# Kernel optimization log

Hardware: AMD Instinct MI355X
Metric: run time of the kernel (lower is better)

## Reference

```python
import jax, jax.numpy as jnp
import numpy as np

EMBED = 2048
HEADS = 32
HEAD_DIM = EMBED // HEADS
Q_BITS = 4
Q_MAX = 2 ** (Q_BITS - 1) - 1  # 7
DECOMP = 8
CHUNK = 256


def _sym_qdq(x, scale):
    # sym_quant followed by sym_dequant (float32 math, clamp to [-8, 7])
    s = jnp.clip(jnp.abs(scale), 1e-9, None)
    return jnp.clip(jnp.round(x / s), -(Q_MAX + 1), Q_MAX) * s


def _quant_weight(w):
    # per-output-channel symmetric int4 quant-dequant of weight [out, in]
    w = w.astype(jnp.float32)
    s = jnp.max(jnp.abs(w), axis=-1, keepdims=True) / Q_MAX
    return _sym_qdq(w, s)


def _chunk_decompose(x2d):
    """Tender chunked activation quantization.
    Splits rows into chunks of CHUNK, subtracts per-chunk channel bias,
    groups channels into DECOMP scale groups by their column max, and
    applies per-group int4 quant-dequant. Vectorized over the DECOMP groups
    (the masks partition channels, so a per-channel scale gather is exact).
    """
    T, H = x2d.shape
    chunks = (T + CHUNK - 1) // CHUNK
    pad = chunks * CHUNK - T
    xp = jnp.pad(x2d, ((0, pad), (0, 0))).reshape(chunks, CHUNK, H).astype(jnp.float32)
    ch_bias = (jnp.max(xp, axis=1, keepdims=True) + jnp.min(xp, axis=1, keepdims=True)) / 2
    xz = xp - ch_bias                                   # [chunks, CHUNK, H]
    tmax = jnp.max(jnp.abs(xz), axis=(1, 2))            # [chunks]
    cmax = jnp.max(jnp.abs(xz), axis=1)                 # [chunks, H]
    # thresholds t_i = tmax / 2^(DECOMP-1-i), ascending in i
    thr = tmax[:, None] / (2.0 ** jnp.arange(DECOMP - 1, -1, -1, dtype=jnp.float32))
    # group index: i=0 if cmax<=t0, else first i with t_{i-1} < cmax <= t_i
    idx = jnp.sum(cmax[:, :, None] > thr[:, None, : DECOMP - 1], axis=-1)  # [chunks, H]
    scale = tmax[:, None] / (2.0 ** (DECOMP - 1 - idx).astype(jnp.float32)) / Q_MAX
    result = _sym_qdq(xz, scale[:, None, :])            # [chunks, CHUNK, H]
    return result, ch_bias, T


def reference(hidden_states, q_weight, k_weight, v_weight, o_weight,
              q_bias, k_bias, v_bias, o_bias):
    bsz, tgt, H = hidden_states.shape
    # int4 dequantized weights, transposed for right-multiply
    WQ = _quant_weight(q_weight).T
    WK = _quant_weight(k_weight).T
    WV = _quant_weight(v_weight).T
    WO = _quant_weight(o_weight).T

    result, ch_bias, n = _chunk_decompose(hidden_states.reshape(bsz * tgt, H))

    def proj(w_orig, w_dq_t, b):
        # bias-corrected dequant GEMM: per-chunk channel bias uses the
        # ORIGINAL (fp) weight, quantized residual uses the int4 weight
        y = result @ w_dq_t + ch_bias @ w_orig.astype(jnp.float32).T
        return y.reshape(-1, H)[:n] + b

    scaling = HEAD_DIM ** -0.5
    Q = (proj(q_weight, WQ, q_bias) * scaling).reshape(bsz, tgt, HEADS, HEAD_DIM)
    K = proj(k_weight, WK, k_bias).reshape(bsz, tgt, HEADS, HEAD_DIM)
    V = proj(v_weight, WV, v_bias).reshape(bsz, tgt, HEADS, HEAD_DIM)

    # quant_mha == False path: plain attention
    attn = jnp.einsum('bqhd,bkhd->bhqk', Q, K)
    probs = jax.nn.softmax(attn, axis=-1)
    ctx = jnp.einsum('bhqk,bkhd->bqhd', probs, V).reshape(bsz * tgt, H)

    # output projection through the same chunked quant pipeline
    r2, cb2, n2 = _chunk_decompose(ctx)
    out = (r2 @ WO + cb2 @ o_weight.astype(jnp.float32).T).reshape(-1, H)[:n2] + o_bias
    return out.reshape(bsz, tgt, H)


def setup_inputs() -> dict:
    key = jax.random.key(0)
    ks = jax.random.split(key, 10)
    B, T = 2, 1024
    inp = {
        'hidden_states': jax.random.normal(ks[0], (B, T, EMBED), dtype=jnp.float32),
        'q_weight': jax.random.normal(ks[1], (EMBED, EMBED), dtype=jnp.float32) * 0.02,
        'k_weight': jax.random.normal(ks[2], (EMBED, EMBED), dtype=jnp.float32) * 0.02,
        'v_weight': jax.random.normal(ks[3], (EMBED, EMBED), dtype=jnp.float32) * 0.02,
        'o_weight': jax.random.normal(ks[4], (EMBED, EMBED), dtype=jnp.float32) * 0.02,
        'q_bias': jax.random.normal(ks[5], (EMBED,), dtype=jnp.float32) * 0.02,
        'k_bias': jax.random.normal(ks[6], (EMBED,), dtype=jnp.float32) * 0.02,
        'v_bias': jax.random.normal(ks[7], (EMBED,), dtype=jnp.float32) * 0.02,
        'o_bias': jax.random.normal(ks[8], (EMBED,), dtype=jnp.float32) * 0.02,
    }
    return inp
```

## Files before the change

### kernel.cpp

```cpp
#include <hip/hip_runtime.h>
#include <hip/hip_bf16.h>

typedef unsigned short u16;
typedef __attribute__((ext_vector_type(8))) short bs8;
typedef __attribute__((ext_vector_type(4))) float fx4;
typedef __attribute__((ext_vector_type(4))) float f4_t;

#define HDIM 2048
#define NCH 8

__device__ inline u16 f2bf(float f) {
  __hip_bfloat16 h = __float2bfloat16(f);
  return __builtin_bit_cast(u16, h);
}
__device__ inline float bf2f(u16 u) {
  __hip_bfloat16 h = __builtin_bit_cast(__hip_bfloat16, u);
  return __bfloat162float(h);
}
__device__ inline float pow2i(int e) {
  return __builtin_bit_cast(float, (unsigned)((127 + e) << 23));
}
__device__ inline void gld_lds16(const void* g, void* l) {
  __builtin_amdgcn_global_load_lds((const __attribute__((address_space(1))) void*)g,
                                   (__attribute__((address_space(3))) void*)l, 16, 0, 0);
}

__global__ __launch_bounds__(256) void k_wquant_cbw(
    const float* __restrict__ w0, const float* __restrict__ w1,
    const float* __restrict__ w2, const float* __restrict__ bias,
    u16* __restrict__ wq, float* __restrict__ sw, float* __restrict__ cbw,
    int NC) {
  int o = blockIdx.x, t = threadIdx.x;
  const float* w = (o < 2048) ? w0 : ((o < 4096) ? w1 : w2);
  const float* wrow = w + (size_t)(o & 2047) * HDIM;
  const f4_t* row4 = (const f4_t*)wrow;
  f4_t x0 = row4[2 * t], x1 = row4[2 * t + 1];
  float am = 0.f;
#pragma unroll
  for (int j = 0; j < 4; j++) { am = fmaxf(am, fabsf(x0[j])); am = fmaxf(am, fabsf(x1[j])); }
#pragma unroll
  for (int m = 1; m < 64; m <<= 1) am = fmaxf(am, __shfl_xor(am, m));
  __shared__ float red[4];
  if ((t & 63) == 0) red[t >> 6] = am;
  __syncthreads();
  am = fmaxf(fmaxf(red[0], red[1]), fmaxf(red[2], red[3]));
  float s = fmaxf(am / 7.0f, 1e-9f);
  if (t == 0) sw[o] = s;
  bs8 ov;
#pragma unroll
  for (int j = 0; j < 4; j++) {
    float q0 = fminf(fmaxf(rintf(x0[j] / s), -8.f), 7.f);
    float q1 = fminf(fmaxf(rintf(x1[j] / s), -8.f), 7.f);
    ov[j]     = (short)f2bf(q0);
    ov[j + 4] = (short)f2bf(q1);
  }
  ((bs8*)(wq + (size_t)o * HDIM))[t] = ov;
  float acc[NCH];
#pragma unroll
  for (int c = 0; c < NCH; c++) {
    const f4_t* bc = (const f4_t*)(bias + (size_t)c * HDIM);
    f4_t b0 = bc[2 * t], b1 = bc[2 * t + 1];
    float a = 0.f;
#pragma unroll
    for (int j = 0; j < 4; j++) a += x0[j] * b0[j] + x1[j] * b1[j];
    acc[c] = a;
  }
  __shared__ float redc[NCH][4];
#pragma unroll
  for (int c = 0; c < NCH; c++) {
    float a = acc[c];
#pragma unroll
    for (int m = 1; m < 64; m <<= 1) a += __shfl_xor(a, m);
    if ((t & 63) == 0) redc[c][t >> 6] = a;
  }
  __syncthreads();
  if (t < NCH) cbw[t * NC + o] = redc[t][0] + redc[t][1] + redc[t][2] + redc[t][3];
}

__global__ __launch_bounds__(256) void k_stats(const float* __restrict__ x,
                                               float* __restrict__ biasO,
                                               float* __restrict__ cmaxO) {
  int ch = blockIdx.x >> 3;
  int c = ((blockIdx.x & 7) << 8) + threadIdx.x;
  const float* base = x + (size_t)ch * 256 * HDIM + c;
  float mx = -1e30f, mn = 1e30f;
  for (int r = 0; r < 256; r++) { float v = base[(size_t)r * HDIM]; mx = fmaxf(mx, v); mn = fminf(mn, v); }
  float bi = (mx + mn) * 0.5f;
  biasO[ch * HDIM + c] = bi;
  cmaxO[ch * HDIM + c] = fmaxf(mx - bi, bi - mn);
}

__global__ __launch_bounds__(256) void k_tscale(const float* __restrict__ cmax,
                                                float* __restrict__ scaleO,
                                                float* __restrict__ e2O,
                                                float* __restrict__ tcO) {
  int ch = blockIdx.x, t = threadIdx.x;
  const float* cr = cmax + ch * HDIM;
  float v[8];
  float mx = 0.f;
#pragma unroll
  for (int i = 0; i < 8; i++) { v[i] = cr[i * 256 + t]; mx = fmaxf(mx, v[i]); }
#pragma unroll
  for (int m = 1; m < 64; m <<= 1) mx = fmaxf(mx, __shfl_xor(mx, m));
  __shared__ float red[4];
  __shared__ float tms;
  if ((t & 63) == 0) red[t >> 6] = mx;
  __syncthreads();
  if (t == 0) tms = fmaxf(fmaxf(red[0], red[1]), fmaxf(red[2], red[3]));
  __syncthreads();
  float tmax = tms;
  if (t == 0) tcO[ch] = (tmax / 7.0f) * pow2i(-7);
#pragma unroll
  for (int i = 0; i < 8; i++) {
    int idx = 0;
#pragma unroll
    for (int k = 0; k < 7; k++) idx += (v[i] > tmax * pow2i(k - 7)) ? 1 : 0;
    float s = (tmax * pow2i(idx - 7)) / 7.0f;
    scaleO[ch * HDIM + i * 256 + t] = fmaxf(s, 1e-9f);
    e2O[ch * HDIM + i * 256 + t] = pow2i(idx);
  }
}

__global__ __launch_bounds__(256) void k_qdq(const float* __restrict__ x,
                                             const float* __restrict__ bias,
                                             const float* __restrict__ scale,
                                             const float* __restrict__ e2,
                                             u16* __restrict__ out) {
  int row = blockIdx.x, t = threadIdx.x;
  int ch = row >> 8;
  const f4_t* xr = (const f4_t*)(x + (size_t)row * HDIM);
  const f4_t* br = (const f4_t*)(bias + (size_t)ch * HDIM);
  const f4_t* sr = (const f4_t*)(scale + (size_t)ch * HDIM);
  const f4_t* er = (const f4_t*)(e2 + (size_t)ch * HDIM);
  f4_t x0 = xr[2 * t], x1 = xr[2 * t + 1];
  f4_t b0 = br[2 * t], b1 = br[2 * t + 1];
  f4_t s0 = sr[2 * t], s1 = sr[2 * t + 1];
  f4_t e0 = er[2 * t], e1 = er[2 * t + 1];
  bs8 ov;
#pragma unroll
  for (int j = 0; j < 4; j++) {
    float q0 = fminf(fmaxf(rintf((x0[j] - b0[j]) / s0[j]), -8.f), 7.f);
    ov[j] = (short)f2bf(q0 * e0[j]);
    float q1 = fminf(fmaxf(rintf((x1[j] - b1[j]) / s1[j]), -8.f), 7.f);
    ov[j + 4] = (short)f2bf(q1 * e1[j]);
  }
  ((bs8*)(out + (size_t)row * HDIM))[t] = ov;
}

__global__ __launch_bounds__(256) void k_gemm(
    const u16* __restrict__ A, const u16* __restrict__ B,
    float* __restrict__ o0, float* __restrict__ o1, float* __restrict__ o2,
    const float* __restrict__ cbw, int NC,
    const float* __restrict__ bb0, const float* __restrict__ bb1,
    const float* __restrict__ bb2,
    const float* __restrict__ tc, const float* __restrict__ sw,
    float scl0, float scl1, float scl2) {
  __shared__ u16 smA[128 * 32];
  __shared__ u16 smB[128 * 32];
  int tid = threadIdx.x;
  int wave = tid >> 6, lane = tid & 63;
  int wr = wave >> 1, wc = wave & 1;
  int row0 = blockIdx.y * 128, col0 = blockIdx.x * 128;
  int mat = col0 >> 11;
  float* out = (mat == 0) ? o0 : ((mat == 1) ? o1 : o2);
  const float* bias = (mat == 0) ? bb0 : ((mat == 1) ? bb1 : bb2);
  float scl = (mat == 0) ? scl0 : ((mat == 1) ? scl1 : scl2);
  int chunk = row0 >> 8;
  fx4 zz = {0.f, 0.f, 0.f, 0.f};
  fx4 acc[4][4];
#pragma unroll
  for (int m = 0; m < 4; m++)
#pragma unroll
    for (int n = 0; n < 4; n++) acc[m][n] = zz;

  int offB = wave * 1024 + lane * 16;
  int sr0 = offB >> 6;
  int sr1 = sr0 + 64;
  int sk = (lane & 3) << 3;
  char* ldsA0 = (char*)smA + wave * 1024;
  char* ldsA1 = (char*)smA + 4096 + wave * 1024;
  char* ldsB0 = (char*)smB + wave * 1024;
  char* ldsB1 = (char*)smB + 4096 + wave * 1024;
  const u16* Ab = A + (size_t)row0 * HDIM;
  const u16* Bb = B + (size_t)col0 * HDIM;

  int arow = wr * 64 + (lane & 15);
  int brow = wc * 64 + (lane & 15);
  int kByte = (lane >> 4) << 4;

  for (int kt = 0; kt < HDIM / 32; kt++) {
    int kb = kt * 32 + sk;
    gld_lds16(Ab + (size_t)sr0 * HDIM + kb, ldsA0);
    gld_lds16(Ab + (size_t)sr1 * HDIM + kb, ldsA1);
    gld_lds16(Bb + (size_t)sr0 * HDIM + kb, ldsB0);
    gld_lds16(Bb + (size_t)sr1 * HDIM + kb, ldsB1);
    __syncthreads();
    bs8 af[4], bfr[4];
#pragma unroll
    for (int m = 0; m < 4; m++)
      af[m] = *(const bs8*)((const char*)smA + (size_t)((arow + m * 16) * 64 + kByte));
#pragma unroll
    for (int n = 0; n < 4; n++)
      bfr[n] = *(const bs8*)((const char*)smB + (size_t)((brow + n * 16) * 64 + kByte));
#pragma unroll
    for (int m = 0; m < 4; m++)
#pragma unroll
      for (int n = 0; n < 4; n++)
        acc[m][n] = __builtin_amdgcn_mfma_f32_16x16x32_bf16(af[m], bfr[n], acc[m][n], 0, 0, 0);
    __syncthreads();
  }
  float tcv = tc[chunk];
  int colb = col0 + wc * 64 + (lane & 15);
  int rowb = row0 + wr * 64 + ((lane >> 4) << 2);
#pragma unroll
  for (int m = 0; m < 4; m++) {
#pragma unroll
    for (int n = 0; n < 4; n++) {
      int colg = colb + n * 16;
      int colL = colg - (mat << 11);
      float sc = tcv * sw[colg];
      float cb = cbw[chunk * NC + colg] + bias[colL];
#pragma unroll
      for (int j = 0; j < 4; j++) {
        int row = rowb + m * 16 + j;
        out[(size_t)row * HDIM + colL] = (acc[m][n][j] * sc + cb) * scl;
      }
    }
  }
}

__global__ __launch_bounds__(256) void k_gemm_sk(const u16* __restrict__ A,
                                                 const u16* __restrict__ B,
                                                 float* __restrict__ pbuf) {
  __shared__ u16 smA[128 * 32];
  __shared__ u16 smB[128 * 32];
  int tid = threadIdx.x;
  int wave = tid >> 6, lane = tid & 63;
  int wr = wave >> 1, wc = wave & 1;
  int row0 = blockIdx.y * 128, col0 = blockIdx.x * 128;
  int z = blockIdx.z;
  float* out = pbuf + (size_t)z * HDIM * HDIM;
  fx4 zz = {0.f, 0.f, 0.f, 0.f};
  fx4 acc[4][4];
#pragma unroll
  for (int m = 0; m < 4; m++)
#pragma unroll
    for (int n = 0; n < 4; n++) acc[m][n] = zz;

  int offB = wave * 1024 + lane * 16;
  int sr0 = offB >> 6;
  int sr1 = sr0 + 64;
  int sk = (lane & 3) << 3;
  char* ldsA0 = (char*)smA + wave * 1024;
  char* ldsA1 = (char*)smA + 4096 + wave * 1024;
  char* ldsB0 = (char*)smB + wave * 1024;
  char* ldsB1 = (char*)smB + 4096 + wave * 1024;
  const u16* Ab = A + (size_t)row0 * HDIM;
  const u16* Bb = B + (size_t)col0 * HDIM;

  int arow = wr * 64 + (lane & 15);
  int brow = wc * 64 + (lane & 15);
  int kByte = (lane >> 4) << 4;

  for (int kt = z * 32; kt < z * 32 + 32; kt++) {
    int kb = kt * 32 + sk;
    gld_lds16(Ab + (size_t)sr0 * HDIM + kb, ldsA0);
    gld_lds16(Ab + (size_t)sr1 * HDIM + kb, ldsA1);
    gld_lds16(Bb + (size_t)sr0 * HDIM + kb, ldsB0);
    gld_lds16(Bb + (size_t)sr1 * HDIM + kb, ldsB1);
    __syncthreads();
    bs8 af[4], bfr[4];
#pragma unroll
    for (int m = 0; m < 4; m++)
      af[m] = *(const bs8*)((const char*)smA + (size_t)((arow + m * 16) * 64 + kByte));
#pragma unroll
    for (int n = 0; n < 4; n++)
      bfr[n] = *(const bs8*)((const char*)smB + (size_t)((brow + n * 16) * 64 + kByte));
#pragma unroll
    for (int m = 0; m < 4; m++)
#pragma unroll
      for (int n = 0; n < 4; n++)
        acc[m][n] = __builtin_amdgcn_mfma_f32_16x16x32_bf16(af[m], bfr[n], acc[m][n], 0, 0, 0);
    __syncthreads();
  }
  int colb = col0 + wc * 64 + (lane & 15);
  int rowb = row0 + wr * 64 + ((lane >> 4) << 2);
#pragma unroll
  for (int m = 0; m < 4; m++)
#pragma unroll
    for (int n = 0; n < 4; n++)
#pragma unroll
      for (int j = 0; j < 4; j++)
        out[(size_t)(rowb + m * 16 + j) * HDIM + colb + n * 16] = acc[m][n][j];
}

__global__ __launch_bounds__(256) void k_fin(const float* __restrict__ p0,
                                             const float* __restrict__ p1,
                                             const float* __restrict__ cbw,
                                             const float* __restrict__ bias,
                                             const float* __restrict__ tc,
                                             const float* __restrict__ sw,
                                             float* __restrict__ out) {
  int row = blockIdx.x, t = threadIdx.x;
  int chunk = row >> 8;
  float tcv = tc[chunk];
  const f4_t* a = (const f4_t*)(p0 + (size_t)row * HDIM);
  const f4_t* b = (const f4_t*)(p1 + (size_t)row * HDIM);
  f4_t* o = (f4_t*)(out + (size_t)row * HDIM);
#pragma unroll
  for (int u = 0; u < 2; u++) {
    f4_t x = a[2 * t + u], y = b[2 * t + u];
    f4_t r;
#pragma unroll
    for (int j = 0; j < 4; j++) {
      int c = (2 * t + u) * 4 + j;
      float sc = tcv * sw[c];
      float cb = cbw[chunk * HDIM + c] + bias[c];
      r[j] = ((x[j] + y[j]) * sc + cb) * 1.0f;
    }
    o[2 * t + u] = r;
  }
}

__global__ __launch_bounds__(256) void k_split(const float* __restrict__ Kf,
                                               const float* __restrict__ Vf,
                                               u16* __restrict__ Khg,
                                               u16* __restrict__ Klg,
                                               u16* __restrict__ Vhg,
                                               u16* __restrict__ Vlg) {
  __shared__ u16 Th[4096], Tl[4096];
  int t = threadIdx.x;
  int ti = blockIdx.x & 15, h = (blockIdx.x >> 4) & 31, b = blockIdx.x >> 9;
  size_t rowStart = (size_t)b * 1024 + ti * 64;
  int colh = h * 64;
  size_t tbase = ((size_t)((b * 32 + h) * 16 + ti)) * 4096;
  int kr = t >> 2, d0 = (t & 3) << 4;
  int xk = (kr & 7) << 3;
  const float* kp = Kf + (rowStart + kr) * HDIM + colh + d0;
  const float* vp = Vf + (rowStart + kr) * HDIM + colh + d0;
  f4_t kv[4], vv[4];
#pragma unroll
  for (int qd = 0; qd < 4; qd++) { kv[qd] = *(const f4_t*)(kp + 4 * qd); vv[qd] = *(const f4_t*)(vp + 4 * qd); }
  bs8 h0, l0, h1, l1;
#pragma unroll
  for (int j = 0; j < 4; j++) {
    float x = kv[0][j]; u16 hh = f2bf(x); h0[j] = (short)hh; l0[j] = (short)f2bf(x - bf2f(hh));
    x = kv[1][j]; hh = f2bf(x); h0[j + 4] = (short)hh; l0[j + 4] = (short)f2bf(x - bf2f(hh));
    x = kv[2][j]; hh = f2bf(x); h1[j] = (short)hh; l1[j] = (short)f2bf(x - bf2f(hh));
    x = kv[3][j]; hh = f2bf(x); h1[j + 4] = (short)hh; l1[j + 4] = (short)f2bf(x - bf2f(hh));
  }
  *(bs8*)(Khg + tbase + kr * 64 + (d0 ^ xk)) = h0;
  *(bs8*)(Klg + tbase + kr * 64 + (d0 ^ xk)) = l0;
  *(bs8*)(Khg + tbase + kr * 64 + ((d0 + 8) ^ xk)) = h1;
  *(bs8*)(Klg + tbase + kr * 64 + ((d0 + 8) ^ xk)) = l1;
#pragma unroll
  for (int qd = 0; qd < 4; qd++)
#pragma unroll
    for (int j = 0; j < 4; j++) {
      int d = d0 + 4 * qd + j;
      float x = vv[qd][j]; u16 hh = f2bf(x);
      int vi = d * 64 + (kr ^ ((d & 7) << 3));
      Th[vi] = hh; Tl[vi] = f2bf(x - bf2f(hh));
    }
  __syncthreads();
  *(bs8*)(Vhg + tbase + t * 16) = *(const bs8*)&Th[t * 16];
  *(bs8*)(Vhg + tbase + t * 16 + 8) = *(const bs8*)&Th[t * 16 + 8];
  *(bs8*)(Vlg + tbase + t * 16) = *(const bs8*)&Tl[t * 16];
  *(bs8*)(Vlg + tbase + t * 16 + 8) = *(const bs8*)&Tl[t * 16 + 8];
}

__global__ __launch_bounds__(256) void k_attn(const float* __restrict__ Q,
                                              const u16* __restrict__ Khg,
                                              const u16* __restrict__ Klg,
                                              const u16* __restrict__ Vhg,
                                              const u16* __restrict__ Vlg,
                                              float* __restrict__ O) {
  __shared__ u16 Kh[64 * 64], Kl[64 * 64];
  __shared__ u16 Vh[64 * 64], Vl[64 * 64];
  int tid = threadIdx.x, wave = tid >> 6, lane = tid & 63;
  int l15 = lane & 15, l4 = lane >> 4;
  int lid = blockIdx.x;
  int xcd = lid & 7, jj = lid >> 3;
  int pair = xcd * 8 + (jj >> 4);
  int qt = jj & 15;
  int h = pair & 31, b = pair >> 5;
  size_t rowStart = (size_t)b * 1024;
  int colh = h * 64;
  int qbase = qt * 64 + wave * 16;
  size_t hbase = (size_t)pair * 16 * 4096;
  u16* Phw = &Kh[wave * 1024];
  u16* Plw = &Kl[wave * 1024];

  bs8 qh[2], ql[2];
#pragma unroll
  for (int kk = 0; kk < 2; kk++) {
    const float* qp = Q + (rowStart + qbase + l15) * HDIM + colh + kk * 32 + (l4 << 3);
    f4_t a0 = *(const f4_t*)qp;
    f4_t a1 = *(const f4_t*)(qp + 4);
#pragma unroll
    for (int j = 0; j < 4; j++) {
      float x = a0[j]; u16 hh = f2bf(x);
      qh[kk][j] = (short)hh; ql[kk][j] = (short)f2bf(x - bf2f(hh));
      x = a1[j]; hh = f2bf(x);
      qh[kk][j + 4] = (short)hh; ql[kk][j + 4] = (short)f2bf(x - bf2f(hh));
    }
  }

  fx4 zz = {0.f, 0.f, 0.f, 0.f};
  fx4 oacc[4];
  float mrun[4], lrun[4];
#pragma unroll
  for (int n = 0; n < 4; n++) oacc[n] = zz;
#pragma unroll
  for (int j = 0; j < 4; j++) { mrun[j] = -1e30f; lrun[j] = 0.f; }

  const u16* garr = (wave == 0) ? Khg : (wave == 1) ? Klg : (wave == 2) ? Vhg : Vlg;
  u16* larr = (wave == 0) ? Kh : (wave == 1) ? Kl : (wave == 2) ? Vh : Vl;

  for (int ti = 0; ti < 16; ti++) {
    const u16* gsrc = garr + hbase + (size_t)ti * 4096 + lane * 8;
#pragma unroll
    for (int seg = 0; seg < 8; seg++)
      gld_lds16(gsrc + seg * 512, larr + seg * 512);
    __syncthreads();

    fx4 sf[4];
#pragma unroll
    for (int n = 0; n < 4; n++) sf[n] = zz;
    __builtin_amdgcn_s_setprio(1);
#pragma unroll
    for (int kk = 0; kk < 2; kk++) {
      int colr = kk * 32 + (l4 << 3);
#pragma unroll
      for (int n = 0; n < 4; n++) {
        int row = n * 16 + l15;
        int ko = row * 64 + (colr ^ ((row & 7) << 3));
        bs8 bh = *(const bs8*)&Kh[ko];
        bs8 bl = *(const bs8*)&Kl[ko];
        sf[n] = __builtin_amdgcn_mfma_f32_16x16x32_bf16(ql[kk], bl, sf[n], 0, 0, 0);
        sf[n] = __builtin_amdgcn_mfma_f32_16x16x32_bf16(ql[kk], bh, sf[n], 0, 0, 0);
        sf[n] = __builtin_amdgcn_mfma_f32_16x16x32_bf16(qh[kk], bl, sf[n], 0, 0, 0);
        sf[n] = __builtin_amdgcn_mfma_f32_16x16x32_bf16(qh[kk], bh, sf[n], 0, 0, 0);
      }
    }
    __builtin_amdgcn_s_setprio(0);
    float corr[4];
#pragma unroll
    for (int j = 0; j < 4; j++) {
      float tm = fmaxf(fmaxf(sf[0][j], sf[1][j]), fmaxf(sf[2][j], sf[3][j]));
#pragma unroll
      for (int msk = 1; msk < 16; msk <<= 1) tm = fmaxf(tm, __shfl_xor(tm, msk));
      float mn = fmaxf(mrun[j], tm);
      corr[j] = __expf(mrun[j] - mn);
      mrun[j] = mn;
      float rs = 0.f;
#pragma unroll
      for (int n = 0; n < 4; n++) { float p = __expf(sf[n][j] - mn); sf[n][j] = p; rs += p; }
#pragma unroll
      for (int msk = 1; msk < 16; msk <<= 1) rs += __shfl_xor(rs, msk);
      lrun[j] = lrun[j] * corr[j] + rs;
    }
#pragma unroll
    for (int n = 0; n < 4; n++)
#pragma unroll
      for (int j = 0; j < 4; j++) oacc[n][j] *= corr[j];
    __syncthreads();
#pragma unroll
    for (int n = 0; n < 4; n++)
#pragma unroll
      for (int j = 0; j < 4; j++) {
        float p = sf[n][j];
        u16 hh = f2bf(p);
        int prow = (l4 << 2) + j;
        int pi = prow * 64 + ((n * 16 + l15) ^ ((prow & 7) << 3));
        Phw[pi] = hh;
        Plw[pi] = f2bf(p - bf2f(hh));
      }
    __builtin_amdgcn_s_setprio(1);
#pragma unroll
    for (int kk = 0; kk < 2; kk++) {
      int colr = kk * 32 + (l4 << 3);
      int ao = l15 * 64 + (colr ^ ((l15 & 7) << 3));
      bs8 pah = *(const bs8*)&Phw[ao];
      bs8 pal = *(const bs8*)&Plw[ao];
#pragma unroll
      for (int n = 0; n < 4; n++) {
        int vrow = n * 16 + l15;
        int vo = vrow * 64 + (colr ^ ((vrow & 7) << 3));
        bs8 vh = *(const bs8*)&Vh[vo];
        bs8 vl = *(const bs8*)&Vl[vo];
        oacc[n] = __builtin_amdgcn_mfma_f32_16x16x32_bf16(pal, vl, oacc[n], 0, 0, 0);
        oacc[n] = __builtin_amdgcn_mfma_f32_16x16x32_bf16(pal, vh, oacc[n], 0, 0, 0);
        oacc[n] = __builtin_amdgcn_mfma_f32_16x16x32_bf16(pah, vl, oacc[n], 0, 0, 0);
        oacc[n] = __builtin_amdgcn_mfma_f32_16x16x32_bf16(pah, vh, oacc[n], 0, 0, 0);
      }
    }
    __builtin_amdgcn_s_setprio(0);
    __syncthreads();
  }
#pragma unroll
  for (int n = 0; n < 4; n++)
#pragma unroll
    for (int j = 0; j < 4; j++)
      O[(rowStart + qbase + (l4 << 2) + j) * HDIM +
        colh + n * 16 + l15] = oacc[n][j] / lrun[j];
}

extern "C" void kernel_launch(void* const* d_in, const int* in_sizes, int n_in,
                              void* d_out, int out_size, void* d_ws, size_t ws_size,
                              hipStream_t stream) {
  const float* hs = (const float*)d_in[0];
  const float* qw = (const float*)d_in[1];
  const float* kw = (const float*)d_in[2];
  const float* vw = (const float*)d_in[3];
  const float* ow = (const float*)d_in[4];
  const float* qb = (const float*)d_in[5];
  const float* kb = (const float*)d_in[6];
  const float* vb = (const float*)d_in[7];
  const float* ob = (const float*)d_in[8];

  char* ws = (char*)d_ws;
  const size_t MB = 1u << 20;
  u16* wqQKV = (u16*)(ws + 0 * MB);
  u16* actA  = (u16*)(ws + 24 * MB);
  u16* Khg   = (u16*)(ws + 0 * MB);
  u16* Klg   = (u16*)(ws + 8 * MB);
  u16* Vhg   = (u16*)(ws + 16 * MB);
  u16* Vlg   = (u16*)(ws + 24 * MB);
  float* p01 = (float*)(ws + 0 * MB);
  float* Qf  = (float*)(ws + 32 * MB);
  float* Kf  = (float*)(ws + 48 * MB);
  float* Vf  = (float*)(ws + 64 * MB);
  u16* actA2 = (u16*)(ws + 48 * MB);
  u16* wqO   = (u16*)(ws + 64 * MB);
  float* sm  = (float*)(ws + 80 * MB);
  float* bias1  = sm;
  float* cmax1  = bias1 + NCH * HDIM;
  float* scale1 = cmax1 + NCH * HDIM;
  float* e2_1   = scale1 + NCH * HDIM;
  float* bias2  = e2_1 + NCH * HDIM;
  float* cmax2  = bias2 + NCH * HDIM;
  float* scale2 = cmax2 + NCH * HDIM;
  float* e2_2   = scale2 + NCH * HDIM;
  float* cbwQKV = e2_2 + NCH * HDIM;
  float* swQKV  = cbwQKV + NCH * 3 * HDIM;
  float* cbwO   = swQKV + 3 * HDIM;
  float* swO    = cbwO + NCH * HDIM;
  float* tc1    = swO + HDIM;
  float* tc2    = tc1 + NCH;
  float* ctx = (float*)d_out;

  k_stats<<<64, 256, 0, stream>>>(hs, bias1, cmax1);
  k_tscale<<<8, 256, 0, stream>>>(cmax1, scale1, e2_1, tc1);
  k_qdq<<<2048, 256, 0, stream>>>(hs, bias1, scale1, e2_1, actA);
  k_wquant_cbw<<<6144, 256, 0, stream>>>(qw, kw, vw, bias1, wqQKV, swQKV, cbwQKV, 3 * HDIM);
  k_gemm<<<dim3(48, 16), 256, 0, stream>>>(actA, wqQKV, Qf, Kf, Vf,
                                           cbwQKV, 3 * HDIM, qb, kb, vb,
                                           tc1, swQKV, 0.125f, 1.0f, 1.0f);
  k_split<<<1024, 256, 0, stream>>>(Kf, Vf, Khg, Klg, Vhg, Vlg);
  k_attn<<<1024, 256, 0, stream>>>(Qf, Khg, Klg, Vhg, Vlg, ctx);
  k_stats<<<64, 256, 0, stream>>>(ctx, bias2, cmax2);
  k_tscale<<<8, 256, 0, stream>>>(cmax2, scale2, e2_2, tc2);
  k_qdq<<<2048, 256, 0, stream>>>(ctx, bias2, scale2, e2_2, actA2);
  k_wquant_cbw<<<2048, 256, 0, stream>>>(ow, ow, ow, bias2, wqO, swO, cbwO, HDIM);
  k_gemm_sk<<<dim3(16, 16, 2), 256, 0, stream>>>(actA2, wqO, p01);
  k_fin<<<2048, 256, 0, stream>>>(p01, p01 + (size_t)HDIM * HDIM,
                                  cbwO, ob, tc2, swO, (float*)d_out);
}
```

Before: 313.2 us.

## Transpose attention MFMAs to keep P in registers and drop LDS round-trip

Swaps MFMA operand order so the score tile comes out transposed. Each lane then holds one query row, so the softmax max/sum needs only two cross-lane shuffles, and the per-row state becomes a single scalar. P is repacked into MFMA operand layout with register shuffles instead of being written to LDS, which removes one __syncthreads per tile and the LDS stores and loads. The output becomes a 16-byte vector store per lane. In exchange it adds many __shfl operations, and correctness depends on the shuffle-based repacking matching the MFMA operand layout exactly.

```diff
diff --git a/kernel.cpp b/kernel.cpp
--- a/kernel.cpp
+++ b/kernel.cpp
@@ -2,9 +2,11 @@
 #include <hip/hip_bf16.h>
 
 typedef unsigned short u16;
+typedef unsigned int u32;
 typedef __attribute__((ext_vector_type(8))) short bs8;
 typedef __attribute__((ext_vector_type(4))) float fx4;
 typedef __attribute__((ext_vector_type(4))) float f4_t;
+typedef __attribute__((ext_vector_type(4))) unsigned int u4_t;
 
 #define HDIM 2048
 #define NCH 8
@@ -388,8 +390,6 @@
   int colh = h * 64;
   int qbase = qt * 64 + wave * 16;
   size_t hbase = (size_t)pair * 16 * 4096;
-  u16* Phw = &Kh[wave * 1024];
-  u16* Plw = &Kl[wave * 1024];
 
   bs8 qh[2], ql[2];
 #pragma unroll
@@ -408,14 +408,16 @@
 
   fx4 zz = {0.f, 0.f, 0.f, 0.f};
   fx4 oacc[4];
-  float mrun[4], lrun[4];
+  float mrun = -1e30f, lrun = 0.f;
 #pragma unroll
   for (int n = 0; n < 4; n++) oacc[n] = zz;
-#pragma unroll
-  for (int j = 0; j < 4; j++) { mrun[j] = -1e30f; lrun[j] = 0.f; }
 
   const u16* garr = (wave == 0) ? Khg : (wave == 1) ? Klg : (wave == 2) ? Vhg : Vlg;
   u16* larr = (wave == 0) ? Kh : (wave == 1) ? Kl : (wave == 2) ? Vh : Vl;
+
+  int srcA = l15 + ((lane & 16) << 1);
+  int srcB = srcA + 16;
+  int hiSel = l4 >> 1;
 
   for (int ti = 0; ti < 16; ti++) {
     const u16* gsrc = garr + hbase + (size_t)ti * 4096 + lane * 8;
@@ -437,73 +439,96 @@
         int ko = row * 64 + (colr ^ ((row & 7) << 3));
         bs8 bh = *(const bs8*)&Kh[ko];
         bs8 bl = *(const bs8*)&Kl[ko];
-        sf[n] = __builtin_amdgcn_mfma_f32_16x16x32_bf16(ql[kk], bl, sf[n], 0, 0, 0);
-        sf[n] = __builtin_amdgcn_mfma_f32_16x16x32_bf16(ql[kk], bh, sf[n], 0, 0, 0);
-        sf[n] = __builtin_amdgcn_mfma_f32_16x16x32_bf16(qh[kk], bl, sf[n], 0, 0, 0);
-        sf[n] = __builtin_amdgcn_mfma_f32_16x16x32_bf16(qh[kk], bh, sf[n], 0, 0, 0);
+        sf[n] = __builtin_amdgcn_mfma_f32_16x16x32_bf16(bl, ql[kk], sf[n], 0, 0, 0);
+        sf[n] = __builtin_amdgcn_mfma_f32_16x16x32_bf16(bh, ql[kk], sf[n], 0, 0, 0);
+        sf[n] = __builtin_amdgcn_mfma_f32_16x16x32_bf16(bl, qh[kk], sf[n], 0, 0, 0);
+        sf[n] = __builtin_amdgcn_mfma_f32_16x16x32_bf16(bh, qh[kk], sf[n], 0, 0, 0);
       }
     }
     __builtin_amdgcn_s_setprio(0);
-    float corr[4];
-#pragma unroll
-    for (int j = 0; j < 4; j++) {
-      float tm = fmaxf(fmaxf(sf[0][j], sf[1][j]), fmaxf(sf[2][j], sf[3][j]));
-#pragma unroll
-      for (int msk = 1; msk < 16; msk <<= 1) tm = fmaxf(tm, __shfl_xor(tm, msk));
-      float mn = fmaxf(mrun[j], tm);
-      corr[j] = __expf(mrun[j] - mn);
-      mrun[j] = mn;
-      float rs = 0.f;
-#pragma unroll
-      for (int n = 0; n < 4; n++) { float p = __expf(sf[n][j] - mn); sf[n][j] = p; rs += p; }
-#pragma unroll
-      for (int msk = 1; msk < 16; msk <<= 1) rs += __shfl_xor(rs, msk);
-      lrun[j] = lrun[j] * corr[j] + rs;
-    }
+    float tm = sf[0][0];
 #pragma unroll
     for (int n = 0; n < 4; n++)
 #pragma unroll
-      for (int j = 0; j < 4; j++) oacc[n][j] *= corr[j];
-    __syncthreads();
+      for (int j = 0; j < 4; j++) tm = fmaxf(tm, sf[n][j]);
+    tm = fmaxf(tm, __shfl_xor(tm, 16));
+    tm = fmaxf(tm, __shfl_xor(tm, 32));
+    float mn = fmaxf(mrun, tm);
+    float corr = __expf(mrun - mn);
+    mrun = mn;
+    float rs = 0.f;
 #pragma unroll
     for (int n = 0; n < 4; n++)
 #pragma unroll
-      for (int j = 0; j < 4; j++) {
-        float p = sf[n][j];
-        u16 hh = f2bf(p);
-        int prow = (l4 << 2) + j;
-        int pi = prow * 64 + ((n * 16 + l15) ^ ((prow & 7) << 3));
-        Phw[pi] = hh;
-        Plw[pi] = f2bf(p - bf2f(hh));
+      for (int j = 0; j < 4; j++) { float p = __expf(sf[n][j] - mn); sf[n][j] = p; rs += p; }
+    rs += __shfl_xor(rs, 16);
+    rs += __shfl_xor(rs, 32);
+    lrun = lrun * corr + rs;
+#pragma unroll
+    for (int n = 0; n < 4; n++)
+#pragma unroll
+      for (int j = 0; j < 4; j++) oacc[n][j] *= corr;
+
+    u32 hiw[4][2], low[4][2];
+#pragma unroll
+    for (int n = 0; n < 4; n++) {
+      u16 hh0 = f2bf(sf[n][0]), hh1 = f2bf(sf[n][1]);
+      u16 hh2 = f2bf(sf[n][2]), hh3 = f2bf(sf[n][3]);
+      u16 ll0 = f2bf(sf[n][0] - bf2f(hh0)), ll1 = f2bf(sf[n][1] - bf2f(hh1));
+      u16 ll2 = f2bf(sf[n][2] - bf2f(hh2)), ll3 = f2bf(sf[n][3] - bf2f(hh3));
+      hiw[n][0] = (u32)hh0 | ((u32)hh1 << 16);
+      hiw[n][1] = (u32)hh2 | ((u32)hh3 << 16);
+      low[n][0] = (u32)ll0 | ((u32)ll1 << 16);
+      low[n][1] = (u32)ll2 | ((u32)ll3 << 16);
+    }
+    bs8 ph[2], pl[2];
+#pragma unroll
+    for (int kkv = 0; kkv < 2; kkv++) {
+      u4_t wh, wl;
+#pragma unroll
+      for (int half = 0; half < 2; half++) {
+        int src = half ? srcB : srcA;
+#pragma unroll
+        for (int pr = 0; pr < 2; pr++) {
+          int a0 = __shfl((int)hiw[2 * kkv][pr], src);
+          int a1 = __shfl((int)hiw[2 * kkv + 1][pr], src);
+          wh[half * 2 + pr] = (u32)(hiSel ? a1 : a0);
+          int b0 = __shfl((int)low[2 * kkv][pr], src);
+          int b1 = __shfl((int)low[2 * kkv + 1][pr], src);
+          wl[half * 2 + pr] = (u32)(hiSel ? b1 : b0);
+        }
       }
+      ph[kkv] = __builtin_bit_cast(bs8, wh);
+      pl[kkv] = __builtin_bit_cast(bs8, wl);
+    }
+
     __builtin_amdgcn_s_setprio(1);
 #pragma unroll
-    for (int kk = 0; kk < 2; kk++) {
-      int colr = kk * 32 + (l4 << 3);
-      int ao = l15 * 64 + (colr ^ ((l15 & 7) << 3));
-      bs8 pah = *(const bs8*)&Phw[ao];
-      bs8 pal = *(const bs8*)&Plw[ao];
+    for (int kkv = 0; kkv < 2; kkv++) {
+      int colr = kkv * 32 + (l4 << 3);
 #pragma unroll
       for (int n = 0; n < 4; n++) {
         int vrow = n * 16 + l15;
         int vo = vrow * 64 + (colr ^ ((vrow & 7) << 3));
         bs8 vh = *(const bs8*)&Vh[vo];
         bs8 vl = *(const bs8*)&Vl[vo];
-        oacc[n] = __builtin_amdgcn_mfma_f32_16x16x32_bf16(pal, vl, oacc[n], 0, 0, 0);
-        oacc[n] = __builtin_amdgcn_mfma_f32_16x16x32_bf16(pal, vh, oacc[n], 0, 0, 0);
-        oacc[n] = __builtin_amdgcn_mfma_f32_16x16x32_bf16(pah, vl, oacc[n], 0, 0, 0);
-        oacc[n] = __builtin_amdgcn_mfma_f32_16x16x32_bf16(pah, vh, oacc[n], 0, 0, 0);
+        oacc[n] = __builtin_amdgcn_mfma_f32_16x16x32_bf16(vl, pl[kkv], oacc[n], 0, 0, 0);
+        oacc[n] = __builtin_amdgcn_mfma_f32_16x16x32_bf16(vh, pl[kkv], oacc[n], 0, 0, 0);
+        oacc[n] = __builtin_amdgcn_mfma_f32_16x16x32_bf16(vl, ph[kkv], oacc[n], 0, 0, 0);
+        oacc[n] = __builtin_amdgcn_mfma_f32_16x16x32_bf16(vh, ph[kkv], oacc[n], 0, 0, 0);
       }
     }
     __builtin_amdgcn_s_setprio(0);
     __syncthreads();
   }
-#pragma unroll
-  for (int n = 0; n < 4; n++)
-#pragma unroll
-    for (int j = 0; j < 4; j++)
-      O[(rowStart + qbase + (l4 << 2) + j) * HDIM +
-        colh + n * 16 + l15] = oacc[n][j] / lrun[j];
+  size_t token = rowStart + qbase + l15;
+#pragma unroll
+  for (int n = 0; n < 4; n++) {
+    f4_t r;
+#pragma unroll
+    for (int j = 0; j < 4; j++) r[j] = oacc[n][j] / lrun;
+    *(f4_t*)(O + token * HDIM + colh + n * 16 + (l4 << 2)) = r;
+  }
 }
 
 extern "C" void kernel_launch(void* const* d_in, const int* in_sizes, int n_in,
```

New measurement: 294.7 us. 1.06x faster.
